# Performance work log

Hardware: AMD Instinct MI355X
Metric: run time of the kernel (lower is better)

## Reference

```python
import jax, jax.numpy as jnp
import numpy as np
from jax import lax

B, NV, W, E, D = 1024, 96, 128, 64, 64

PNAMES = ['enc_Wih','enc_Whh','enc_bih','enc_bhh','enc_lv','enc_lw','enc_lwb','enc_lu','enc_lub',
          'dec_Wih','dec_Whh','dec_bih','dec_bhh','dec_lv','dec_lw','dec_lwb','dec_lu','dec_lub',
          'dec_lp','dec_lpb','dec_ly','dec_lyb']


def setup_inputs() -> dict:
    key = jax.random.key(0)
    ks = jax.random.split(key, 24)
    n = lambda k, shp, s=0.05: jax.random.normal(k, shp, dtype=jnp.float32) * s
    return {
        'x': n(ks[0], (B, NV, W), 1.0),
        'enc_Wih': n(ks[1], (4*E, NV)), 'enc_Whh': n(ks[2], (4*E, E)),
        'enc_bih': n(ks[3], (4*E,)), 'enc_bhh': n(ks[4], (4*E,)),
        'enc_lv': n(ks[5], (1, W)),
        'enc_lw': n(ks[6], (W, 2*E)), 'enc_lwb': n(ks[7], (W,)),
        'enc_lu': n(ks[8], (W, W)), 'enc_lub': n(ks[9], (W,)),
        'dec_Wih': n(ks[10], (4*D, 1)), 'dec_Whh': n(ks[11], (4*D, D)),
        'dec_bih': n(ks[12], (4*D,)), 'dec_bhh': n(ks[13], (4*D,)),
        'dec_lv': n(ks[14], (1, D)),
        'dec_lw': n(ks[15], (E, 2*D)), 'dec_lwb': n(ks[16], (E,)),
        'dec_lu': n(ks[17], (E, E)), 'dec_lub': n(ks[18], (E,)),
        'dec_lp': n(ks[19], (1, D+1)), 'dec_lpb': n(ks[20], (1,)),
        'dec_ly': n(ks[21], (1, 2*D)), 'dec_lyb': n(ks[22], (1,)),
        'target': 7,
    }


def lstm_cell(xt, h, c, Wih, Whh, bih, bhh):
    # PyTorch LSTM gate order: i, f, g, o
    g = xt @ Wih.T + bih + h @ Whh.T + bhh
    i, f, gg, o = jnp.split(g, 4, axis=-1)
    c = jax.nn.sigmoid(f) * c + jax.nn.sigmoid(i) * jnp.tanh(gg)
    h = jax.nn.sigmoid(o) * jnp.tanh(c)
    return h, c


def darnn(x, target, p):
    y = x[:, target, :]                                             # [B, W]
    # ---------- encoder (input attention over variables) ----------
    u_e = jnp.einsum('bnw,ow->bno', x, p['enc_lu']) + p['enc_lub']  # [B,NV,W]
    xs = jnp.moveaxis(x, 2, 0)                                      # [W,B,NV]

    def enc_step(carry, xt):
        h, c = carry
        w_out = jnp.concatenate([h, c], axis=1) @ p['enc_lw'].T + p['enc_lwb']      # [B,W]
        scores = jnp.einsum('bnw,w->bn', jnp.tanh(w_out[:, None, :] + u_e), p['enc_lv'][0])
        alpha = jax.nn.softmax(scores, axis=1)                       # softmax over variables
        x_tilde = alpha * xt                                         # [B,NV]
        h, c = lstm_cell(x_tilde, h, c, p['enc_Wih'], p['enc_Whh'], p['enc_bih'], p['enc_bhh'])
        return (h, c), h

    z = jnp.zeros((B, E), jnp.float32)
    _, h_seq = lax.scan(enc_step, (z, z), xs)                        # [W,B,E]

    # ---------- decoder (temporal attention over encoder states) ----------
    u_d = h_seq @ p['dec_lu'].T + p['dec_lub']                       # [W,B,E]

    def dec_step(carry, y_prev):
        h, c = carry
        w_out = jnp.concatenate([h, c], axis=1) @ p['dec_lw'].T + p['dec_lwb']      # [B,E]
        v = jnp.einsum('wbe,e->wb', jnp.tanh(w_out[None] + u_d), p['dec_lv'][0])    # [W,B]
        beta = jax.nn.softmax(v, axis=0)                             # softmax over time
        context = jnp.einsum('wb,wbe->be', beta, h_seq)              # [B,E]
        y_tilde = jnp.concatenate([y_prev[:, None], context], axis=1) @ p['dec_lp'].T + p['dec_lpb']  # [B,1]
        h, c = lstm_cell(y_tilde, h, c, p['dec_Wih'], p['dec_Whh'], p['dec_bih'], p['dec_bhh'])
        return (h, c), None

    zd = jnp.zeros((B, D), jnp.float32)
    (h, c), _ = lax.scan(dec_step, (zd, zd), y[:, :W-1].T)           # steps i=1..W-1 use y[:, i-1]
    return (jnp.concatenate([h, c], axis=1) @ p['dec_ly'].T + p['dec_lyb'])[:, 0]


def reference(x, enc_Wih, enc_Whh, enc_bih, enc_bhh, enc_lv, enc_lw, enc_lwb, enc_lu, enc_lub,
              dec_Wih, dec_Whh, dec_bih, dec_bhh, dec_lv, dec_lw, dec_lwb, dec_lu, dec_lub,
              dec_lp, dec_lpb, dec_ly, dec_lyb, target):
    vals = (enc_Wih, enc_Whh, enc_bih, enc_bhh, enc_lv, enc_lw, enc_lwb, enc_lu, enc_lub,
            dec_Wih, dec_Whh, dec_bih, dec_bhh, dec_lv, dec_lw, dec_lwb, dec_lu, dec_lub,
            dec_lp, dec_lpb, dec_ly, dec_lyb)
    p = dict(zip(PNAMES, vals))
    return darnn(x, target, p)
```

## Files before the change

### kernel.cpp

```cpp
#include <hip/hip_runtime.h>

#define NB 1024
#define NV 96
#define WW 128
#define EE 64
#define DD 64

typedef _Float16 h2t __attribute__((ext_vector_type(2)));
typedef float f2t __attribute__((ext_vector_type(2)));
typedef float f4t __attribute__((ext_vector_type(4)));

#define CLOG 2.885390081777927f
#define L2E  1.4426950408889634f

__device__ __forceinline__ float fdot2(h2t a, h2t b, float c) {
    return __builtin_amdgcn_fdot2(a, b, c, false);
}
__device__ __forceinline__ h2t pk2(float a, float b) {
    h2t r; r.x = (_Float16)a; r.y = (_Float16)b; return r;
}
__device__ __forceinline__ h2t bch(float f) { return __builtin_bit_cast(h2t, f); }
__device__ __forceinline__ float bcf(h2t p) { return __builtin_bit_cast(float, p); }
__device__ __forceinline__ float ex2(float x) { return __builtin_amdgcn_exp2f(x); }
__device__ __forceinline__ float rcp_(float x) { return __builtin_amdgcn_rcpf(x); }
__device__ __forceinline__ float sig_c(float x) { return rcp_(1.f + ex2(-x * L2E)); }
__device__ __forceinline__ float tanh_c(float x) { return 1.f - 2.f * rcp_(ex2(x * CLOG) + 1.f); }
__device__ __forceinline__ float wsum(float v) {
#pragma unroll
    for (int o = 32; o; o >>= 1) v += __shfl_xor(v, o, 64);
    return v;
}

#define DOT4(V, WR, B, ACC) do { \
    ACC = fdot2(bch((V).x), (WR)[(B) + 0], ACC); \
    ACC = fdot2(bch((V).y), (WR)[(B) + 1], ACC); \
    ACC = fdot2(bch((V).z), (WR)[(B) + 2], ACC); \
    ACC = fdot2(bch((V).w), (WR)[(B) + 3], ACC); } while (0)

#define DOT4W(V, W4, ACC) do { \
    ACC = fdot2(bch((V).x), bch((W4).x), ACC); \
    ACC = fdot2(bch((V).y), bch((W4).y), ACC); \
    ACC = fdot2(bch((V).z), bch((W4).z), ACC); \
    ACC = fdot2(bch((V).w), bch((W4).w), ACC); } while (0)

template<bool HSG>
__global__ __launch_bounds__(256, 2)
void darnn_kernel(
    const float* __restrict__ x,
    const float* __restrict__ eWih, const float* __restrict__ eWhh,
    const float* __restrict__ ebih, const float* __restrict__ ebhh,
    const float* __restrict__ elv,  const float* __restrict__ elw,
    const float* __restrict__ elwb, const float* __restrict__ elu,
    const float* __restrict__ elub,
    const float* __restrict__ dWih, const float* __restrict__ dWhh,
    const float* __restrict__ dbih, const float* __restrict__ dbhh,
    const float* __restrict__ dlv,  const float* __restrict__ dlw,
    const float* __restrict__ dlwb, const float* __restrict__ dlu,
    const float* __restrict__ dlub, const float* __restrict__ dlp,
    const float* __restrict__ dlpb, const float* __restrict__ dly,
    const float* __restrict__ dlyb, const int* __restrict__ tgtp,
    h2t* __restrict__ hsg_all,
    float* __restrict__ out)
{
    __shared__ __align__(16) h2t  s_pool[96 * 64];
    __shared__ __align__(16) h2t  s_hseq2[HSG ? 1 : WW][32];
    __shared__ __align__(16) f4t  s_wlv[64];
    __shared__ __align__(16) char s_u2[1024];
    __shared__ __align__(16) float s_soft[128];
    __shared__ __align__(16) h2t  s_hch2[2][64];
    __shared__ __align__(16) f4t  s_spillh[2][256];
    __shared__ __align__(16) f4t  s_spillw[256];

    float* s_wlvf = (float*)s_wlv;
    h2t*  const s_xt  = (h2t*)s_u2;
    float* const s_tmp = (float*)s_u2;

    const int tid  = threadIdx.x;
    const int b    = blockIdx.x;
    const int lane = tid & 63, wq = tid >> 6;
    const int uidx = wq * 16 + (lane >> 2);
    const int jrow = (lane & 3) * 64 + uidx;
    const float* xb = x + (size_t)b * NV * WW;
    h2t* hsgb = HSG ? (hsg_all + (size_t)b * (WW * 32)) : (h2t*)nullptr;

    float c_reg = 0.f;

    if (tid >= 96 && tid < 128) s_soft[tid] = 0.f;
    if (tid < 64) {
        s_hch2[0][tid] = pk2(0.f, 0.f);
        s_wlvf[tid * 4 + 2] = elv[2 * tid];
        s_wlvf[tid * 4 + 3] = elv[2 * tid + 1];
    }

    {
        const int o = tid >> 1, p = tid & 1;
        f4t lu4[16];
        const f4t* lur = (const f4t*)(elu + o * WW + p * 64);
#pragma unroll
        for (int i = 0; i < 16; ++i) lu4[i] = lur[i];
        const float lub_o = elub[o];
        for (int n = 0; n < NV; ++n) {
            const f4t* xr = (const f4t*)(xb + n * WW + p * 64);
            float a = 0.f;
#pragma unroll
            for (int i = 0; i < 16; ++i) {
                f4t v = xr[i], l4 = lu4[i];
                a = fmaf(v.x, l4.x, a); a = fmaf(v.y, l4.y, a);
                a = fmaf(v.z, l4.z, a); a = fmaf(v.w, l4.w, a);
            }
            a += __shfl_xor(a, 1, 64);
            float val = (a + lub_o) * CLOG;
            float vn  = __shfl_xor(val, 2, 64);
            if (!(tid & 3)) s_pool[n * 64 + ((tid >> 2) ^ (n & 31))] = pk2(val, vn);
        }
    }
    __syncthreads();
    __builtin_amdgcn_sched_barrier(0);

    float elvsum;
    {
        const f2t lvp = *(const f2t*)&s_wlvf[(tid & 63) * 4 + 2];
        elvsum = wsum(lvp.x + lvp.y);
    }

    h2t lw_r[32];
    {
        const f2t* r = (const f2t*)(elw + (tid >> 1) * 128 + (tid & 1) * 64);
#pragma unroll
        for (int i = 0; i < 32; ++i) { f2t v = r[i]; lw_r[i] = pk2(v.x, v.y); }
    }
    const float lwb_r = elwb[tid >> 1];
    h2t wih_r[44];
    {
        const f2t* r = (const f2t*)(eWih + jrow * 96);
#pragma unroll
        for (int i = 0; i < 44; ++i) { f2t v = r[i]; wih_r[i] = pk2(v.x, v.y); }
        f4t ws;
        { f2t v = r[44]; ws.x = bcf(pk2(v.x, v.y)); }
        { f2t v = r[45]; ws.y = bcf(pk2(v.x, v.y)); }
        { f2t v = r[46]; ws.z = bcf(pk2(v.x, v.y)); }
        { f2t v = r[47]; ws.w = bcf(pk2(v.x, v.y)); }
        s_spillw[tid] = ws;
    }
    h2t whh_r[24];
    {
        const f2t* r = (const f2t*)(eWhh + jrow * 64);
#pragma unroll
        for (int i = 0; i < 24; ++i) { f2t v = r[i]; whh_r[i] = pk2(v.x, v.y); }
        f4t w0, w1;
        { f2t v = r[24]; w0.x = bcf(pk2(v.x, v.y)); }
        { f2t v = r[25]; w0.y = bcf(pk2(v.x, v.y)); }
        { f2t v = r[26]; w0.z = bcf(pk2(v.x, v.y)); }
        { f2t v = r[27]; w0.w = bcf(pk2(v.x, v.y)); }
        { f2t v = r[28]; w1.x = bcf(pk2(v.x, v.y)); }
        { f2t v = r[29]; w1.y = bcf(pk2(v.x, v.y)); }
        { f2t v = r[30]; w1.z = bcf(pk2(v.x, v.y)); }
        { f2t v = r[31]; w1.w = bcf(pk2(v.x, v.y)); }
        s_spillh[0][tid] = w0;
        s_spillh[1][tid] = w1;
    }
    const float bsum_r = ebih[jrow] + ebhh[jrow];
    __builtin_amdgcn_sched_barrier(0);

#pragma unroll 1
    for (int t = 0; t < WW; ++t) {
        const int pp = t & 1;
        float xv = 0.f;
        if (!(tid & 1) && tid < 192) xv = xb[(tid >> 1) * WW + t];
        {
            const f4t* hc4 = (const f4t*)&s_hch2[pp][(tid & 1) * 32];
            float a = 0.f;
#pragma unroll
            for (int i = 0; i < 8; ++i) { f4t v = hc4[i]; DOT4(v, lw_r, 4 * i, a); }
            a += __shfl_xor(a, 1, 64);
            float wo = (a + lwb_r) * CLOG;
            float wn = __shfl_xor(wo, 2, 64);
            if (!(tid & 3)) { f2t st = {wo, wn}; *(f2t*)&s_wlvf[(tid >> 2) * 4] = st; }
        }
        __syncthreads();
        float prod = 0.f;
        if (tid < 192) {
            const int n = tid >> 1, sw = n & 31;
            const h2t* uer = s_pool + n * 64;
            float a = 0.f;
#pragma unroll
            for (int j = 0; j < 32; ++j) {
                const int wp = (tid & 1) * 32 + j;
                f4t wl = s_wlv[wp];
                h2t u  = uer[wp ^ sw];
                float r0 = rcp_(ex2(wl.x + (float)u.x) + 1.f);
                float r1 = rcp_(ex2(wl.y + (float)u.y) + 1.f);
                a = fmaf(wl.z, r0, a);
                a = fmaf(wl.w, r1, a);
            }
            a += __shfl_xor(a, 1, 64);
            if (!(tid & 1)) {
                float e = ex2((elvsum - 2.f * a) * L2E);
                prod = e * xv;
                s_soft[n] = e;
            }
        }
        __syncthreads();
        if (tid < 192) {
            const int l = tid & 63;
            float sm = s_soft[l] + s_soft[64 + l];
            sm = wsum(sm);
            float inv = rcp_(sm);
            float p1 = __shfl_xor(prod, 2, 64);
            if (!(tid & 3)) s_xt[tid >> 2] = pk2(prod * inv, p1 * inv);
        }
        __syncthreads();
        {
            float gv = bsum_r;
            const f4t* xt4 = (const f4t*)s_xt;
#pragma unroll
            for (int i = 0; i < 11; ++i) { f4t v = xt4[i]; DOT4(v, wih_r, 4 * i, gv); }
            { f4t v = xt4[11]; f4t w = s_spillw[tid]; DOT4W(v, w, gv); }
            const f4t* h4 = (const f4t*)&s_hch2[pp][0];
#pragma unroll
            for (int i = 0; i < 6; ++i) { f4t v = h4[i]; DOT4(v, whh_r, 4 * i, gv); }
            { f4t v = h4[6]; f4t w = s_spillh[0][tid]; DOT4W(v, w, gv); }
            { f4t v = h4[7]; f4t w = s_spillh[1][tid]; DOT4W(v, w, gv); }
            const int base = lane & ~3;
            float gi = __shfl(gv, base, 64);
            float gf = __shfl(gv, base + 1, 64);
            float g2 = __shfl(gv, base + 2, 64);
            float go = __shfl(gv, base + 3, 64);
            float c = sig_c(gf) * c_reg + sig_c(gi) * tanh_c(g2);
            float h = sig_c(go) * tanh_c(c);
            c_reg = c;
            float hn = __shfl_xor(h, 4, 64);
            float cn = __shfl_xor(c, 4, 64);
            if (!(lane & 7)) {
                const int k = wq * 8 + (lane >> 3);
                s_hch2[pp ^ 1][k]      = pk2(h, hn);
                s_hch2[pp ^ 1][32 + k] = pk2(c, cn);
                if constexpr (HSG) hsgb[t * 32 + k] = pk2(h, hn);
                else               s_hseq2[t][k ^ (t & 31)] = pk2(h, hn);
            }
        }
        __syncthreads();
    }

    {
        const int e2h = tid & 31;
        h2t du0[32], du1[32];
        {
            const f4t* p0 = (const f4t*)(dlu + (2 * e2h) * 64);
            const f4t* p1 = (const f4t*)(dlu + (2 * e2h + 1) * 64);
#pragma unroll
            for (int i = 0; i < 16; ++i) {
                f4t v0 = p0[i], v1 = p1[i];
                du0[2 * i] = pk2(v0.x, v0.y); du0[2 * i + 1] = pk2(v0.z, v0.w);
                du1[2 * i] = pk2(v1.x, v1.y); du1[2 * i + 1] = pk2(v1.z, v1.w);
            }
        }
        const float b0 = dlub[2 * e2h], b1 = dlub[2 * e2h + 1];
#pragma unroll 1
        for (int pass = 0; pass < 16; ++pass) {
            const int w = pass * 8 + (tid >> 5);
            float a0 = b0, a1 = b1;
            if constexpr (HSG) {
                const f4t* hr = (const f4t*)(hsgb + w * 32);
#pragma unroll
                for (int i = 0; i < 8; ++i) {
                    f4t v = hr[i];
                    DOT4(v, du0, 4 * i, a0);
                    DOT4(v, du1, 4 * i, a1);
                }
            } else {
                const int sww = w & 31;
#pragma unroll
                for (int i = 0; i < 32; ++i) {
                    h2t hp = s_hseq2[w][i ^ sww];
                    a0 = fdot2(hp, du0[i], a0);
                    a1 = fdot2(hp, du1[i], a1);
                }
            }
            s_pool[w * 32 + (e2h ^ (w & 31))] = pk2(a0 * CLOG, a1 * CLOG);
        }
    }
    __builtin_amdgcn_sched_barrier(0);

    const int tgt = tgtp[0];
    if (tid < 32) {
        s_wlvf[tid * 4 + 2] = dlv[2 * tid];
        s_wlvf[tid * 4 + 3] = dlv[2 * tid + 1];
    }
    if (tid < 64) s_hch2[0][tid] = pk2(0.f, 0.f);
    float dlvsum;
    { float v = dlv[tid & 63]; dlvsum = wsum(v); }
    h2t dlw_r[16];
    {
        const f2t* r = (const f2t*)(dlw + (tid >> 2) * 128 + (tid & 3) * 32);
#pragma unroll
        for (int i = 0; i < 16; ++i) { f2t v = r[i]; dlw_r[i] = pk2(v.x, v.y); }
    }
    const float dlwb_r = dlwb[tid >> 2];
    h2t dwhh_r[32];
    {
        const f2t* r = (const f2t*)(dWhh + jrow * 64);
#pragma unroll
        for (int i = 0; i < 32; ++i) { f2t v = r[i]; dwhh_r[i] = pk2(v.x, v.y); }
    }
    const float dwih_r  = dWih[jrow];
    const float dbsum_r = dbih[jrow] + dbhh[jrow];
    const float lp0     = dlp[0];
    const float lp1_r   = dlp[1 + (tid & 63)];
    const float lpb     = dlpb[0];
    c_reg = 0.f;
    float h_reg = 0.f;
    __syncthreads();

#pragma unroll 1
    for (int s = 0; s < WW - 1; ++s) {
        const int pp = s & 1;
        const float ys = xb[(size_t)tgt * WW + s];
        {
            const f4t* hc4 = (const f4t*)&s_hch2[pp][(tid & 3) * 16];
            float a = 0.f;
#pragma unroll
            for (int i = 0; i < 4; ++i) { f4t v = hc4[i]; DOT4(v, dlw_r, 4 * i, a); }
            a += __shfl_xor(a, 1, 64);
            a += __shfl_xor(a, 2, 64);
            float wo = (a + dlwb_r) * CLOG;
            float wn = __shfl_xor(wo, 4, 64);
            if (!(tid & 7)) { f2t st = {wo, wn}; *(f2t*)&s_wlvf[(tid >> 3) * 4] = st; }
        }
        __syncthreads();
        {
            const int w = tid >> 1, sw = w & 31;
            const h2t* udr = s_pool + w * 32;
            float a = 0.f;
#pragma unroll
            for (int j = 0; j < 16; ++j) {
                const int ep = (tid & 1) * 16 + j;
                f4t wl = s_wlv[ep];
                h2t u  = udr[ep ^ sw];
                float r0 = rcp_(ex2(wl.x + (float)u.x) + 1.f);
                float r1 = rcp_(ex2(wl.y + (float)u.y) + 1.f);
                a = fmaf(wl.z, r0, a);
                a = fmaf(wl.w, r1, a);
            }
            a += __shfl_xor(a, 1, 64);
            if (!(tid & 1)) s_soft[w] = ex2((dlvsum - 2.f * a) * L2E);
        }
        __syncthreads();
        float inv;
        {
            const int l = tid & 63;
            float sm = s_soft[l] + s_soft[64 + l];
            sm = wsum(sm);
            inv = rcp_(sm);
            const int e2 = tid & 31, pg = tid >> 5;
            float a0 = 0.f, a1 = 0.f;
#pragma unroll
            for (int j = 0; j < 16; ++j) {
                const int w = pg * 16 + j;
                float bw = s_soft[w];
                h2t hp;
                if constexpr (HSG) hp = hsgb[w * 32 + e2];
                else               hp = s_hseq2[w][e2 ^ (w & 31)];
                a0 = fmaf(bw, (float)hp.x, a0);
                a1 = fmaf(bw, (float)hp.y, a1);
            }
            a0 += __shfl_xor(a0, 32, 64);
            a1 += __shfl_xor(a1, 32, 64);
            if ((tid & 63) < 32) { f2t st = {a0, a1}; *(f2t*)&s_tmp[wq * 64 + e2 * 2] = st; }
        }
        __syncthreads();
        {
            const int l = tid & 63;
            float ctx = s_tmp[l] + s_tmp[64 + l] + s_tmp[128 + l] + s_tmp[192 + l];
            float term = ctx * inv * lp1_r;
            term = wsum(term);
            float yt = fmaf(ys, lp0, term + lpb);
            float gv = fmaf(yt, dwih_r, dbsum_r);
            const f4t* h4 = (const f4t*)&s_hch2[pp][0];
#pragma unroll
            for (int i = 0; i < 8; ++i) { f4t v = h4[i]; DOT4(v, dwhh_r, 4 * i, gv); }
            const int base = l & ~3;
            float gi = __shfl(gv, base, 64);
            float gf = __shfl(gv, base + 1, 64);
            float g2 = __shfl(gv, base + 2, 64);
            float go = __shfl(gv, base + 3, 64);
            float c = sig_c(gf) * c_reg + sig_c(gi) * tanh_c(g2);
            float h = sig_c(go) * tanh_c(c);
            c_reg = c; h_reg = h;
            float hn = __shfl_xor(h, 4, 64);
            float cn = __shfl_xor(c, 4, 64);
            if (!(l & 7)) {
                const int k = wq * 8 + (l >> 3);
                s_hch2[pp ^ 1][k]      = pk2(h, hn);
                s_hch2[pp ^ 1][32 + k] = pk2(c, cn);
            }
        }
        __syncthreads();
    }

    {
        float term = 0.f;
        if (!(lane & 3)) term = h_reg * dly[uidx] + c_reg * dly[64 + uidx];
        term = wsum(term);
        if (lane == 0) s_tmp[wq] = term;
    }
    __syncthreads();
    if (tid == 0) out[b] = s_tmp[0] + s_tmp[1] + s_tmp[2] + s_tmp[3] + dlyb[0];
}

extern "C" void kernel_launch(void* const* d_in, const int* in_sizes, int n_in,
                              void* d_out, int out_size, void* d_ws, size_t ws_size,
                              hipStream_t stream) {
    (void)in_sizes; (void)n_in; (void)out_size;
    const float* x    = (const float*)d_in[0];
    const float* eWih = (const float*)d_in[1];
    const float* eWhh = (const float*)d_in[2];
    const float* ebih = (const float*)d_in[3];
    const float* ebhh = (const float*)d_in[4];
    const float* elv  = (const float*)d_in[5];
    const float* elw  = (const float*)d_in[6];
    const float* elwb = (const float*)d_in[7];
    const float* elu  = (const float*)d_in[8];
    const float* elub = (const float*)d_in[9];
    const float* dWih = (const float*)d_in[10];
    const float* dWhh = (const float*)d_in[11];
    const float* dbih = (const float*)d_in[12];
    const float* dbhh = (const float*)d_in[13];
    const float* dlv  = (const float*)d_in[14];
    const float* dlw  = (const float*)d_in[15];
    const float* dlwb = (const float*)d_in[16];
    const float* dlu  = (const float*)d_in[17];
    const float* dlub = (const float*)d_in[18];
    const float* dlp  = (const float*)d_in[19];
    const float* dlpb = (const float*)d_in[20];
    const float* dly  = (const float*)d_in[21];
    const float* dlyb = (const float*)d_in[22];
    const int*   tgt  = (const int*)d_in[23];
    float* out = (float*)d_out;

    const size_t need = (size_t)NB * WW * 32 * sizeof(h2t);
    if (d_ws && ws_size >= need) {
        darnn_kernel<true><<<NB, 256, 0, stream>>>(
            x, eWih, eWhh, ebih, ebhh, elv, elw, elwb, elu, elub,
            dWih, dWhh, dbih, dbhh, dlv, dlw, dlwb, dlu, dlub,
            dlp, dlpb, dly, dlyb, tgt, (h2t*)d_ws, out);
    } else {
        darnn_kernel<false><<<NB, 256, 0, stream>>>(
            x, eWih, eWhh, ebih, ebhh, elv, elw, elwb, elu, elub,
            dWih, dWhh, dbih, dbhh, dlv, dlw, dlwb, dlu, dlub,
            dlp, dlpb, dly, dlyb, tgt, (h2t*)nullptr, out);
    }
}
```

Measured before the change: 1.815 ms.

## Process two batch elements per block to amortize weights and syncs

Adds a new kernel in which each 256-thread block handles two batch samples instead of one, launching NB/2 blocks. Register-resident weights and every barrier are shared across the two samples, and the independent A/B dot products interleave to give more instruction-level parallelism in the serial recurrence. This halves the block count, so fewer waves run concurrently on the GPU. It also raises register pressure and LDS use (a larger u_e buffer and more weight spill slots), which could limit occupancy.

```diff
diff --git a/kernel.cpp b/kernel.cpp
--- a/kernel.cpp
+++ b/kernel.cpp
@@ -43,9 +43,8 @@
     ACC = fdot2(bch((V).z), bch((W4).z), ACC); \
     ACC = fdot2(bch((V).w), bch((W4).w), ACC); } while (0)
 
-template<bool HSG>
 __global__ __launch_bounds__(256, 2)
-void darnn_kernel(
+void darnn2_kernel(
     const float* __restrict__ x,
     const float* __restrict__ eWih, const float* __restrict__ eWhh,
     const float* __restrict__ ebih, const float* __restrict__ ebhh,
@@ -62,8 +61,480 @@
     h2t* __restrict__ hsg_all,
     float* __restrict__ out)
 {
+    __shared__ __align__(16) h2t  s_ue[96 * 128];
+    __shared__ __align__(16) f4t  s_wo4[64];
+    __shared__ __align__(16) f2t  s_lv[64];
+    __shared__ __align__(16) f2t  s_soft2[128];
+    __shared__ __align__(16) char s_u2v[2048];
+    __shared__ __align__(16) h2t  s_hch2[2][2][64];
+    __shared__ __align__(16) f4t  s_spw[4][256];
+    __shared__ __align__(16) f4t  s_sph[2][256];
+    __shared__ float s_scal[8];
+
+    h2t*  const s_xtA  = (h2t*)s_u2v;
+    h2t*  const s_xtB  = (h2t*)(s_u2v + 1024);
+    f4t*  const s_tmp4 = (f4t*)s_u2v;
+
+    const int tid  = threadIdx.x;
+    const int b    = blockIdx.x;
+    const int lane = tid & 63, wq = tid >> 6;
+    const int uidx = wq * 16 + (lane >> 2);
+    const int jrow = (lane & 3) * 64 + uidx;
+    const float* xbA = x + (size_t)(2 * b) * NV * WW;
+    const float* xbB = xbA + NV * WW;
+    h2t* hsgP = hsg_all + (size_t)b * (WW * 64);
+
+    float c_regA = 0.f, c_regB = 0.f;
+
+    if (tid >= 96 && tid < 128) { f2t z = {0.f, 0.f}; s_soft2[tid] = z; }
+    if (tid < 64) {
+        s_hch2[0][0][tid] = pk2(0.f, 0.f);
+        s_hch2[0][1][tid] = pk2(0.f, 0.f);
+        f2t lv = { elv[2 * tid], elv[2 * tid + 1] };
+        s_lv[tid] = lv;
+    }
+
+    {
+        const int o = tid >> 1, p = tid & 1;
+        f4t lu4[16];
+        const f4t* lur = (const f4t*)(elu + o * WW + p * 64);
+#pragma unroll
+        for (int i = 0; i < 16; ++i) lu4[i] = lur[i];
+        const float lub_o = elub[o];
+        for (int n = 0; n < NV; ++n) {
+            const f4t* xrA = (const f4t*)(xbA + n * WW + p * 64);
+            const f4t* xrB = (const f4t*)(xbB + n * WW + p * 64);
+            float aA = 0.f, aB = 0.f;
+#pragma unroll
+            for (int i = 0; i < 16; ++i) {
+                f4t vA = xrA[i], vB = xrB[i], l4 = lu4[i];
+                aA = fmaf(vA.x, l4.x, aA); aA = fmaf(vA.y, l4.y, aA);
+                aA = fmaf(vA.z, l4.z, aA); aA = fmaf(vA.w, l4.w, aA);
+                aB = fmaf(vB.x, l4.x, aB); aB = fmaf(vB.y, l4.y, aB);
+                aB = fmaf(vB.z, l4.z, aB); aB = fmaf(vB.w, l4.w, aB);
+            }
+            aA += __shfl_xor(aA, 1, 64);
+            aB += __shfl_xor(aB, 1, 64);
+            float valA = (aA + lub_o) * CLOG;
+            float valB = (aB + lub_o) * CLOG;
+            float vnA = __shfl_xor(valA, 2, 64);
+            float vnB = __shfl_xor(valB, 2, 64);
+            if (!(tid & 3)) {
+                const int k = tid >> 2;
+                f2t st = { bcf(pk2(valA, vnA)), bcf(pk2(valB, vnB)) };
+                *(f2t*)&s_ue[n * 128 + ((k ^ (n & 31)) << 1)] = st;
+            }
+        }
+    }
+    __syncthreads();
+    __builtin_amdgcn_sched_barrier(0);
+
+    float elvsum;
+    { f2t lv = s_lv[lane]; elvsum = wsum(lv.x + lv.y); }
+
+    h2t lw_r[32];
+    {
+        const f2t* r = (const f2t*)(elw + (tid >> 1) * 128 + (tid & 1) * 64);
+#pragma unroll
+        for (int i = 0; i < 32; ++i) { f2t v = r[i]; lw_r[i] = pk2(v.x, v.y); }
+    }
+    const float lwb_r = elwb[tid >> 1];
+    h2t wih_r[32];
+    {
+        const f2t* r = (const f2t*)(eWih + jrow * 96);
+#pragma unroll
+        for (int i = 0; i < 32; ++i) { f2t v = r[i]; wih_r[i] = pk2(v.x, v.y); }
+#pragma unroll
+        for (int g = 0; g < 4; ++g) {
+            f4t ws;
+            { f2t v = r[32 + 4*g];     ws.x = bcf(pk2(v.x, v.y)); }
+            { f2t v = r[33 + 4*g];     ws.y = bcf(pk2(v.x, v.y)); }
+            { f2t v = r[34 + 4*g];     ws.z = bcf(pk2(v.x, v.y)); }
+            { f2t v = r[35 + 4*g];     ws.w = bcf(pk2(v.x, v.y)); }
+            s_spw[g][tid] = ws;
+        }
+    }
+    h2t whh_r[24];
+    {
+        const f2t* r = (const f2t*)(eWhh + jrow * 64);
+#pragma unroll
+        for (int i = 0; i < 24; ++i) { f2t v = r[i]; whh_r[i] = pk2(v.x, v.y); }
+#pragma unroll
+        for (int g = 0; g < 2; ++g) {
+            f4t ws;
+            { f2t v = r[24 + 4*g];     ws.x = bcf(pk2(v.x, v.y)); }
+            { f2t v = r[25 + 4*g];     ws.y = bcf(pk2(v.x, v.y)); }
+            { f2t v = r[26 + 4*g];     ws.z = bcf(pk2(v.x, v.y)); }
+            { f2t v = r[27 + 4*g];     ws.w = bcf(pk2(v.x, v.y)); }
+            s_sph[g][tid] = ws;
+        }
+    }
+    const float bsum_r = ebih[jrow] + ebhh[jrow];
+    __builtin_amdgcn_sched_barrier(0);
+
+#pragma unroll 1
+    for (int t = 0; t < WW; ++t) {
+        const int pp = t & 1;
+        float xvA = 0.f, xvB = 0.f;
+        if (!(tid & 1) && tid < 192) {
+            const int n = tid >> 1;
+            xvA = xbA[n * WW + t]; xvB = xbB[n * WW + t];
+        }
+        {
+            const f4t* hcA = (const f4t*)&s_hch2[pp][0][(tid & 1) * 32];
+            const f4t* hcB = (const f4t*)&s_hch2[pp][1][(tid & 1) * 32];
+            float aA = 0.f, aB = 0.f;
+#pragma unroll
+            for (int i = 0; i < 8; ++i) {
+                f4t vA = hcA[i], vB = hcB[i];
+                DOT4(vA, lw_r, 4 * i, aA);
+                DOT4(vB, lw_r, 4 * i, aB);
+            }
+            aA += __shfl_xor(aA, 1, 64); aB += __shfl_xor(aB, 1, 64);
+            float woA = (aA + lwb_r) * CLOG, woB = (aB + lwb_r) * CLOG;
+            float wnA = __shfl_xor(woA, 2, 64), wnB = __shfl_xor(woB, 2, 64);
+            if (!(tid & 3)) { f4t st = {woA, wnA, woB, wnB}; s_wo4[tid >> 2] = st; }
+        }
+        __syncthreads();
+        float prodA = 0.f, prodB = 0.f;
+        if (tid < 192) {
+            const int n = tid >> 1, part = tid & 1, sw = n & 31;
+            const h2t* uer = s_ue + n * 128;
+            float aA = 0.f, aB = 0.f;
+#pragma unroll
+            for (int j = 0; j < 32; ++j) {
+                const int wp = part * 32 + j;
+                f4t w4 = s_wo4[wp];
+                f2t lv = s_lv[wp];
+                f2t up = *(const f2t*)&uer[(wp ^ sw) << 1];
+                h2t uA = bch(up.x), uB = bch(up.y);
+                float r0A = rcp_(ex2(w4.x + (float)uA.x) + 1.f);
+                float r1A = rcp_(ex2(w4.y + (float)uA.y) + 1.f);
+                float r0B = rcp_(ex2(w4.z + (float)uB.x) + 1.f);
+                float r1B = rcp_(ex2(w4.w + (float)uB.y) + 1.f);
+                aA = fmaf(lv.x, r0A, aA); aA = fmaf(lv.y, r1A, aA);
+                aB = fmaf(lv.x, r0B, aB); aB = fmaf(lv.y, r1B, aB);
+            }
+            aA += __shfl_xor(aA, 1, 64); aB += __shfl_xor(aB, 1, 64);
+            if (!(tid & 1)) {
+                float eA = ex2((elvsum - 2.f * aA) * L2E);
+                float eB = ex2((elvsum - 2.f * aB) * L2E);
+                prodA = eA * xvA; prodB = eB * xvB;
+                f2t st = {eA, eB}; s_soft2[tid >> 1] = st;
+            }
+        }
+        __syncthreads();
+        if (tid < 192) {
+            const int l = tid & 63;
+            f2t s0 = s_soft2[l], s1 = s_soft2[64 + l];
+            float smA = s0.x + s1.x, smB = s0.y + s1.y;
+#pragma unroll
+            for (int o = 32; o; o >>= 1) {
+                smA += __shfl_xor(smA, o, 64);
+                smB += __shfl_xor(smB, o, 64);
+            }
+            float invA = rcp_(smA), invB = rcp_(smB);
+            float p1A = __shfl_xor(prodA, 2, 64), p1B = __shfl_xor(prodB, 2, 64);
+            if (!(tid & 3)) {
+                s_xtA[tid >> 2] = pk2(prodA * invA, p1A * invA);
+                s_xtB[tid >> 2] = pk2(prodB * invB, p1B * invB);
+            }
+        }
+        __syncthreads();
+        {
+            float gA = bsum_r, gB = bsum_r;
+            const f4t* xtA4 = (const f4t*)s_xtA;
+            const f4t* xtB4 = (const f4t*)s_xtB;
+#pragma unroll
+            for (int i = 0; i < 8; ++i) {
+                f4t vA = xtA4[i], vB = xtB4[i];
+                DOT4(vA, wih_r, 4 * i, gA);
+                DOT4(vB, wih_r, 4 * i, gB);
+            }
+#pragma unroll
+            for (int g = 0; g < 4; ++g) {
+                f4t w = s_spw[g][tid];
+                f4t vA = xtA4[8 + g], vB = xtB4[8 + g];
+                DOT4W(vA, w, gA); DOT4W(vB, w, gB);
+            }
+            const f4t* hA4 = (const f4t*)&s_hch2[pp][0][0];
+            const f4t* hB4 = (const f4t*)&s_hch2[pp][1][0];
+#pragma unroll
+            for (int i = 0; i < 6; ++i) {
+                f4t vA = hA4[i], vB = hB4[i];
+                DOT4(vA, whh_r, 4 * i, gA);
+                DOT4(vB, whh_r, 4 * i, gB);
+            }
+#pragma unroll
+            for (int g = 0; g < 2; ++g) {
+                f4t w = s_sph[g][tid];
+                f4t vA = hA4[6 + g], vB = hB4[6 + g];
+                DOT4W(vA, w, gA); DOT4W(vB, w, gB);
+            }
+            const int base = lane & ~3;
+            float giA = __shfl(gA, base, 64),     giB = __shfl(gB, base, 64);
+            float gfA = __shfl(gA, base + 1, 64), gfB = __shfl(gB, base + 1, 64);
+            float g2A = __shfl(gA, base + 2, 64), g2B = __shfl(gB, base + 2, 64);
+            float goA = __shfl(gA, base + 3, 64), goB = __shfl(gB, base + 3, 64);
+            float cA = sig_c(gfA) * c_regA + sig_c(giA) * tanh_c(g2A);
+            float cB = sig_c(gfB) * c_regB + sig_c(giB) * tanh_c(g2B);
+            float hA = sig_c(goA) * tanh_c(cA);
+            float hB = sig_c(goB) * tanh_c(cB);
+            c_regA = cA; c_regB = cB;
+            float hnA = __shfl_xor(hA, 4, 64), cnA = __shfl_xor(cA, 4, 64);
+            float hnB = __shfl_xor(hB, 4, 64), cnB = __shfl_xor(cB, 4, 64);
+            if (!(lane & 7)) {
+                const int k = wq * 8 + (lane >> 3);
+                h2t phA = pk2(hA, hnA), phB = pk2(hB, hnB);
+                s_hch2[pp ^ 1][0][k]      = phA;
+                s_hch2[pp ^ 1][0][32 + k] = pk2(cA, cnA);
+                s_hch2[pp ^ 1][1][k]      = phB;
+                s_hch2[pp ^ 1][1][32 + k] = pk2(cB, cnB);
+                f2t st = { bcf(phA), bcf(phB) };
+                *(f2t*)&hsgP[t * 64 + k * 2] = st;
+            }
+        }
+        __syncthreads();
+    }
+
+    {
+        const int e2h = tid & 31;
+        h2t du0[32], du1[32];
+        {
+            const f4t* p0 = (const f4t*)(dlu + (2 * e2h) * 64);
+            const f4t* p1 = (const f4t*)(dlu + (2 * e2h + 1) * 64);
+#pragma unroll
+            for (int i = 0; i < 16; ++i) {
+                f4t v0 = p0[i], v1 = p1[i];
+                du0[2 * i] = pk2(v0.x, v0.y); du0[2 * i + 1] = pk2(v0.z, v0.w);
+                du1[2 * i] = pk2(v1.x, v1.y); du1[2 * i + 1] = pk2(v1.z, v1.w);
+            }
+        }
+        const float b0 = dlub[2 * e2h], b1 = dlub[2 * e2h + 1];
+#pragma unroll 1
+        for (int pass = 0; pass < 16; ++pass) {
+            const int w = pass * 8 + (tid >> 5);
+            float a0A = b0, a1A = b1, a0B = b0, a1B = b1;
+            const f4t* hr = (const f4t*)(hsgP + w * 64);
+#pragma unroll
+            for (int i = 0; i < 16; ++i) {
+                f4t v = hr[i];
+                a0A = fdot2(bch(v.x), du0[2*i], a0A); a0A = fdot2(bch(v.z), du0[2*i+1], a0A);
+                a1A = fdot2(bch(v.x), du1[2*i], a1A); a1A = fdot2(bch(v.z), du1[2*i+1], a1A);
+                a0B = fdot2(bch(v.y), du0[2*i], a0B); a0B = fdot2(bch(v.w), du0[2*i+1], a0B);
+                a1B = fdot2(bch(v.y), du1[2*i], a1B); a1B = fdot2(bch(v.w), du1[2*i+1], a1B);
+            }
+            f2t st = { bcf(pk2(a0A * CLOG, a1A * CLOG)), bcf(pk2(a0B * CLOG, a1B * CLOG)) };
+            *(f2t*)&s_ue[w * 64 + ((e2h ^ (w & 31)) << 1)] = st;
+        }
+    }
+    __builtin_amdgcn_sched_barrier(0);
+
+    const int tgt = tgtp[0];
+    if (tid < 32) { f2t lv = { dlv[2 * tid], dlv[2 * tid + 1] }; s_lv[tid] = lv; }
+    if (tid < 64) {
+        s_hch2[0][0][tid] = pk2(0.f, 0.f);
+        s_hch2[0][1][tid] = pk2(0.f, 0.f);
+    }
+    float dlvsum;
+    { float v = dlv[lane]; dlvsum = wsum(v); }
+    h2t dlw_r[16];
+    {
+        const f2t* r = (const f2t*)(dlw + (tid >> 2) * 128 + (tid & 3) * 32);
+#pragma unroll
+        for (int i = 0; i < 16; ++i) { f2t v = r[i]; dlw_r[i] = pk2(v.x, v.y); }
+    }
+    const float dlwb_r = dlwb[tid >> 2];
+    h2t dwhh_r[24];
+    {
+        const f2t* r = (const f2t*)(dWhh + jrow * 64);
+#pragma unroll
+        for (int i = 0; i < 24; ++i) { f2t v = r[i]; dwhh_r[i] = pk2(v.x, v.y); }
+#pragma unroll
+        for (int g = 0; g < 2; ++g) {
+            f4t ws;
+            { f2t v = r[24 + 4*g]; ws.x = bcf(pk2(v.x, v.y)); }
+            { f2t v = r[25 + 4*g]; ws.y = bcf(pk2(v.x, v.y)); }
+            { f2t v = r[26 + 4*g]; ws.z = bcf(pk2(v.x, v.y)); }
+            { f2t v = r[27 + 4*g]; ws.w = bcf(pk2(v.x, v.y)); }
+            s_sph[g][tid] = ws;
+        }
+    }
+    const float dwih_r  = dWih[jrow];
+    const float dbsum_r = dbih[jrow] + dbhh[jrow];
+    const float lp0     = dlp[0];
+    const float lp1_r   = dlp[1 + lane];
+    const float lpb     = dlpb[0];
+    c_regA = 0.f; c_regB = 0.f;
+    float h_regA = 0.f, h_regB = 0.f;
+    __syncthreads();
+
+#pragma unroll 1
+    for (int s = 0; s < WW - 1; ++s) {
+        const int pp = s & 1;
+        const float ysA = xbA[(size_t)tgt * WW + s];
+        const float ysB = xbB[(size_t)tgt * WW + s];
+        {
+            const f4t* hcA = (const f4t*)&s_hch2[pp][0][(tid & 3) * 16];
+            const f4t* hcB = (const f4t*)&s_hch2[pp][1][(tid & 3) * 16];
+            float aA = 0.f, aB = 0.f;
+#pragma unroll
+            for (int i = 0; i < 4; ++i) {
+                f4t vA = hcA[i], vB = hcB[i];
+                DOT4(vA, dlw_r, 4 * i, aA);
+                DOT4(vB, dlw_r, 4 * i, aB);
+            }
+            aA += __shfl_xor(aA, 1, 64); aB += __shfl_xor(aB, 1, 64);
+            aA += __shfl_xor(aA, 2, 64); aB += __shfl_xor(aB, 2, 64);
+            float woA = (aA + dlwb_r) * CLOG, woB = (aB + dlwb_r) * CLOG;
+            float wnA = __shfl_xor(woA, 4, 64), wnB = __shfl_xor(woB, 4, 64);
+            if (!(tid & 7)) { f4t st = {woA, wnA, woB, wnB}; s_wo4[tid >> 3] = st; }
+        }
+        __syncthreads();
+        {
+            const int w = tid >> 1, part = tid & 1, sw = w & 31;
+            const h2t* udr = s_ue + w * 64;
+            float aA = 0.f, aB = 0.f;
+#pragma unroll
+            for (int j = 0; j < 16; ++j) {
+                const int ep = part * 16 + j;
+                f4t w4 = s_wo4[ep];
+                f2t lv = s_lv[ep];
+                f2t up = *(const f2t*)&udr[(ep ^ sw) << 1];
+                h2t uA = bch(up.x), uB = bch(up.y);
+                float r0A = rcp_(ex2(w4.x + (float)uA.x) + 1.f);
+                float r1A = rcp_(ex2(w4.y + (float)uA.y) + 1.f);
+                float r0B = rcp_(ex2(w4.z + (float)uB.x) + 1.f);
+                float r1B = rcp_(ex2(w4.w + (float)uB.y) + 1.f);
+                aA = fmaf(lv.x, r0A, aA); aA = fmaf(lv.y, r1A, aA);
+                aB = fmaf(lv.x, r0B, aB); aB = fmaf(lv.y, r1B, aB);
+            }
+            aA += __shfl_xor(aA, 1, 64); aB += __shfl_xor(aB, 1, 64);
+            if (!(tid & 1)) {
+                float eA = ex2((dlvsum - 2.f * aA) * L2E);
+                float eB = ex2((dlvsum - 2.f * aB) * L2E);
+                f2t st = {eA, eB}; s_soft2[w] = st;
+            }
+        }
+        __syncthreads();
+        float invA, invB;
+        {
+            const int l = tid & 63;
+            f2t s0 = s_soft2[l], s1 = s_soft2[64 + l];
+            float smA = s0.x + s1.x, smB = s0.y + s1.y;
+#pragma unroll
+            for (int o = 32; o; o >>= 1) {
+                smA += __shfl_xor(smA, o, 64);
+                smB += __shfl_xor(smB, o, 64);
+            }
+            invA = rcp_(smA); invB = rcp_(smB);
+            const int e2 = tid & 31, pg = tid >> 5;
+            float a0A = 0.f, a1A = 0.f, a0B = 0.f, a1B = 0.f;
+#pragma unroll
+            for (int j = 0; j < 16; ++j) {
+                const int w = pg * 16 + j;
+                f2t be = s_soft2[w];
+                f2t hp = *(const f2t*)&hsgP[w * 64 + e2 * 2];
+                h2t hA = bch(hp.x), hB = bch(hp.y);
+                a0A = fmaf(be.x, (float)hA.x, a0A); a1A = fmaf(be.x, (float)hA.y, a1A);
+                a0B = fmaf(be.y, (float)hB.x, a0B); a1B = fmaf(be.y, (float)hB.y, a1B);
+            }
+            a0A += __shfl_xor(a0A, 32, 64); a1A += __shfl_xor(a1A, 32, 64);
+            a0B += __shfl_xor(a0B, 32, 64); a1B += __shfl_xor(a1B, 32, 64);
+            if ((tid & 63) < 32) { f4t st = {a0A, a1A, a0B, a1B}; s_tmp4[wq * 32 + e2] = st; }
+        }
+        __syncthreads();
+        {
+            const int l = tid & 63;
+            const int eh = l >> 1;
+            f4t p0 = s_tmp4[eh], p1 = s_tmp4[32 + eh], p2 = s_tmp4[64 + eh], p3 = s_tmp4[96 + eh];
+            float ctxA = (l & 1) ? (p0.y + p1.y + p2.y + p3.y) : (p0.x + p1.x + p2.x + p3.x);
+            float ctxB = (l & 1) ? (p0.w + p1.w + p2.w + p3.w) : (p0.z + p1.z + p2.z + p3.z);
+            float termA = ctxA * invA * lp1_r;
+            float termB = ctxB * invB * lp1_r;
+#pragma unroll
+            for (int o = 32; o; o >>= 1) {
+                termA += __shfl_xor(termA, o, 64);
+                termB += __shfl_xor(termB, o, 64);
+            }
+            float ytA = fmaf(ysA, lp0, termA + lpb);
+            float ytB = fmaf(ysB, lp0, termB + lpb);
+            float gA = fmaf(ytA, dwih_r, dbsum_r);
+            float gB = fmaf(ytB, dwih_r, dbsum_r);
+            const f4t* hA4 = (const f4t*)&s_hch2[pp][0][0];
+            const f4t* hB4 = (const f4t*)&s_hch2[pp][1][0];
+#pragma unroll
+            for (int i = 0; i < 6; ++i) {
+                f4t vA = hA4[i], vB = hB4[i];
+                DOT4(vA, dwhh_r, 4 * i, gA);
+                DOT4(vB, dwhh_r, 4 * i, gB);
+            }
+#pragma unroll
+            for (int g = 0; g < 2; ++g) {
+                f4t w = s_sph[g][tid];
+                f4t vA = hA4[6 + g], vB = hB4[6 + g];
+                DOT4W(vA, w, gA); DOT4W(vB, w, gB);
+            }
+            const int base = lane & ~3;
+            float giA = __shfl(gA, base, 64),     giB = __shfl(gB, base, 64);
+            float gfA = __shfl(gA, base + 1, 64), gfB = __shfl(gB, base + 1, 64);
+            float g2A = __shfl(gA, base + 2, 64), g2B = __shfl(gB, base + 2, 64);
+            float goA = __shfl(gA, base + 3, 64), goB = __shfl(gB, base + 3, 64);
+            float cA = sig_c(gfA) * c_regA + sig_c(giA) * tanh_c(g2A);
+            float cB = sig_c(gfB) * c_regB + sig_c(giB) * tanh_c(g2B);
+            float hA = sig_c(goA) * tanh_c(cA);
+            float hB = sig_c(goB) * tanh_c(cB);
+            c_regA = cA; c_regB = cB; h_regA = hA; h_regB = hB;
+            float hnA = __shfl_xor(hA, 4, 64), cnA = __shfl_xor(cA, 4, 64);
+            float hnB = __shfl_xor(hB, 4, 64), cnB = __shfl_xor(cB, 4, 64);
+            if (!(lane & 7)) {
+                const int k = wq * 8 + (lane >> 3);
+                s_hch2[pp ^ 1][0][k]      = pk2(hA, hnA);
+                s_hch2[pp ^ 1][0][32 + k] = pk2(cA, cnA);
+                s_hch2[pp ^ 1][1][k]      = pk2(hB, hnB);
+                s_hch2[pp ^ 1][1][32 + k] = pk2(cB, cnB);
+            }
+        }
+        __syncthreads();
+    }
+
+    {
+        float termA = 0.f, termB = 0.f;
+        if (!(lane & 3)) {
+            termA = h_regA * dly[uidx] + c_regA * dly[64 + uidx];
+            termB = h_regB * dly[uidx] + c_regB * dly[64 + uidx];
+        }
+#pragma unroll
+        for (int o = 32; o; o >>= 1) {
+            termA += __shfl_xor(termA, o, 64);
+            termB += __shfl_xor(termB, o, 64);
+        }
+        if (lane == 0) { s_scal[wq] = termA; s_scal[4 + wq] = termB; }
+    }
+    __syncthreads();
+    if (tid == 0) out[2 * b]     = s_scal[0] + s_scal[1] + s_scal[2] + s_scal[3] + dlyb[0];
+    if (tid == 1) out[2 * b + 1] = s_scal[4] + s_scal[5] + s_scal[6] + s_scal[7] + dlyb[0];
+}
+
+__global__ __launch_bounds__(256, 2)
+void darnn1_kernel(
+    const float* __restrict__ x,
+    const float* __restrict__ eWih, const float* __restrict__ eWhh,
+    const float* __restrict__ ebih, const float* __restrict__ ebhh,
+    const float* __restrict__ elv,  const float* __restrict__ elw,
+    const float* __restrict__ elwb, const float* __restrict__ elu,
+    const float* __restrict__ elub,
+    const float* __restrict__ dWih, const float* __restrict__ dWhh,
+    const float* __restrict__ dbih, const float* __restrict__ dbhh,
+    const float* __restrict__ dlv,  const float* __restrict__ dlw,
+    const float* __restrict__ dlwb, const float* __restrict__ dlu,
+    const float* __restrict__ dlub, const float* __restrict__ dlp,
+    const float* __restrict__ dlpb, const float* __restrict__ dly,
+    const float* __restrict__ dlyb, const int* __restrict__ tgtp,
+    float* __restrict__ out)
+{
     __shared__ __align__(16) h2t  s_pool[96 * 64];
-    __shared__ __align__(16) h2t  s_hseq2[HSG ? 1 : WW][32];
+    __shared__ __align__(16) h2t  s_hseq2[WW][32];
     __shared__ __align__(16) f4t  s_wlv[64];
     __shared__ __align__(16) char s_u2[1024];
     __shared__ __align__(16) float s_soft[128];
@@ -81,7 +552,6 @@
     const int uidx = wq * 16 + (lane >> 2);
     const int jrow = (lane & 3) * 64 + uidx;
     const float* xb = x + (size_t)b * NV * WW;
-    h2t* hsgb = HSG ? (hsg_all + (size_t)b * (WW * 32)) : (h2t*)nullptr;
 
     float c_reg = 0.f;
 
@@ -91,7 +561,6 @@
         s_wlvf[tid * 4 + 2] = elv[2 * tid];
         s_wlvf[tid * 4 + 3] = elv[2 * tid + 1];
     }
-
     {
         const int o = tid >> 1, p = tid & 1;
         f4t lu4[16];
@@ -122,7 +591,6 @@
         const f2t lvp = *(const f2t*)&s_wlvf[(tid & 63) * 4 + 2];
         elvsum = wsum(lvp.x + lvp.y);
     }
-
     h2t lw_r[32];
     {
         const f2t* r = (const f2t*)(elw + (tid >> 1) * 128 + (tid & 1) * 64);
@@ -197,7 +665,7 @@
             if (!(tid & 1)) {
                 float e = ex2((elvsum - 2.f * a) * L2E);
                 prod = e * xv;
-                s_soft[n] = e;
+                s_soft[tid >> 1] = e;
             }
         }
         __syncthreads();
@@ -235,13 +703,11 @@
                 const int k = wq * 8 + (lane >> 3);
                 s_hch2[pp ^ 1][k]      = pk2(h, hn);
                 s_hch2[pp ^ 1][32 + k] = pk2(c, cn);
-                if constexpr (HSG) hsgb[t * 32 + k] = pk2(h, hn);
-                else               s_hseq2[t][k ^ (t & 31)] = pk2(h, hn);
-            }
-        }
-        __syncthreads();
-    }
-
+                s_hseq2[t][k ^ (t & 31)] = pk2(h, hn);
+            }
+        }
+        __syncthreads();
+    }
     {
         const int e2h = tid & 31;
         h2t du0[32], du1[32];
@@ -260,22 +726,12 @@
         for (int pass = 0; pass < 16; ++pass) {
             const int w = pass * 8 + (tid >> 5);
             float a0 = b0, a1 = b1;
-            if constexpr (HSG) {
-                const f4t* hr = (const f4t*)(hsgb + w * 32);
-#pragma unroll
-                for (int i = 0; i < 8; ++i) {
-                    f4t v = hr[i];
-                    DOT4(v, du0, 4 * i, a0);
-                    DOT4(v, du1, 4 * i, a1);
-                }
-            } else {
-                const int sww = w & 31;
-#pragma unroll
-                for (int i = 0; i < 32; ++i) {
-                    h2t hp = s_hseq2[w][i ^ sww];
-                    a0 = fdot2(hp, du0[i], a0);
-                    a1 = fdot2(hp, du1[i], a1);
-                }
+            const int sww = w & 31;
+#pragma unroll
+            for (int i = 0; i < 32; ++i) {
+                h2t hp = s_hseq2[w][i ^ sww];
+                a0 = fdot2(hp, du0[i], a0);
+                a1 = fdot2(hp, du1[i], a1);
             }
             s_pool[w * 32 + (e2h ^ (w & 31))] = pk2(a0 * CLOG, a1 * CLOG);
         }
@@ -358,9 +814,7 @@
             for (int j = 0; j < 16; ++j) {
                 const int w = pg * 16 + j;
                 float bw = s_soft[w];
-                h2t hp;
-                if constexpr (HSG) hp = hsgb[w * 32 + e2];
-                else               hp = s_hseq2[w][e2 ^ (w & 31)];
+                h2t hp = s_hseq2[w][e2 ^ (w & 31)];
                 a0 = fmaf(bw, (float)hp.x, a0);
                 a1 = fmaf(bw, (float)hp.y, a1);
             }
@@ -379,7 +833,7 @@
             const f4t* h4 = (const f4t*)&s_hch2[pp][0];
 #pragma unroll
             for (int i = 0; i < 8; ++i) { f4t v = h4[i]; DOT4(v, dwhh_r, 4 * i, gv); }
-            const int base = l & ~3;
+            const int base = lane & ~3;
             float gi = __shfl(gv, base, 64);
             float gf = __shfl(gv, base + 1, 64);
             float g2 = __shfl(gv, base + 2, 64);
@@ -389,15 +843,14 @@
             c_reg = c; h_reg = h;
             float hn = __shfl_xor(h, 4, 64);
             float cn = __shfl_xor(c, 4, 64);
-            if (!(l & 7)) {
-                const int k = wq * 8 + (l >> 3);
+            if (!(lane & 7)) {
+                const int k = wq * 8 + (lane >> 3);
                 s_hch2[pp ^ 1][k]      = pk2(h, hn);
                 s_hch2[pp ^ 1][32 + k] = pk2(c, cn);
             }
         }
         __syncthreads();
     }
-
     {
         float term = 0.f;
         if (!(lane & 3)) term = h_reg * dly[uidx] + c_reg * dly[64 + uidx];
@@ -440,14 +893,14 @@
 
     const size_t need = (size_t)NB * WW * 32 * sizeof(h2t);
     if (d_ws && ws_size >= need) {
-        darnn_kernel<true><<<NB, 256, 0, stream>>>(
+        darnn2_kernel<<<NB / 2, 256, 0, stream>>>(
             x, eWih, eWhh, ebih, ebhh, elv, elw, elwb, elu, elub,
             dWih, dWhh, dbih, dbhh, dlv, dlw, dlwb, dlu, dlub,
             dlp, dlpb, dly, dlyb, tgt, (h2t*)d_ws, out);
     } else {
-        darnn_kernel<false><<<NB, 256, 0, stream>>>(
+        darnn1_kernel<<<NB, 256, 0, stream>>>(
             x, eWih, eWhh, ebih, ebhh, elv, elw, elwb, elu, elub,
             dWih, dWhh, dbih, dbhh, dlv, dlw, dlwb, dlu, dlub,
-            dlp, dlpb, dly, dlyb, tgt, (h2t*)nullptr, out);
+            dlp, dlpb, dly, dlyb, tgt, out);
     }
 }
```

Measured after the change: 1.714 ms. 1.06x faster.
